# Kernel tuning notes

Measured on AMD Instinct MI355X. Metric: run time of the kernel, lower is better.

The kernel has to match this reference:

```python
import jax, jax.numpy as jnp
import numpy as np

B, S, D, H, OUT = 64, 512, 128, 512, 24


def _linear_params(key, out_dim, in_dim, dtype=jnp.float32):
    kw, kb = jax.random.split(key)
    bound = 1.0 / np.sqrt(in_dim)
    w = jax.random.uniform(kw, (out_dim, in_dim), dtype, -bound, bound)
    b = jax.random.uniform(kb, (out_dim,), dtype, -bound, bound)
    return w, b


def setup_inputs() -> dict:
    key = jax.random.key(0)
    ks = jax.random.split(key, 12)
    inp = {"x": jax.random.normal(ks[0], (B, S, D), jnp.float32)}
    # layer 0 gates: Linear(D+H, H); layer 1 gates: Linear(2H, H)
    names = ["f", "i", "o", "g"]
    for li, in_dim in enumerate([D + H, 2 * H]):
        for gi, n in enumerate(names):
            w, b = _linear_params(ks[1 + li * 4 + gi], H, in_dim)
            inp[f"w{n}{li}"] = w
            inp[f"b{n}{li}"] = b
    inp["fc1_w"], inp["fc1_b"] = _linear_params(ks[9], H, H)
    inp["fc2_w"], inp["fc2_b"] = _linear_params(ks[10], OUT, H)
    return inp


def _cell(inp, h, c, wf, bf, wi, bi, wo, bo, wg, bg):
    comb = jnp.concatenate([inp, h], axis=1)          # [B, in+H]
    f = jax.nn.sigmoid(comb @ wf.T + bf)
    i = jax.nn.sigmoid(comb @ wi.T + bi)
    g = jnp.tanh(comb @ wg.T + bg)
    c = f * c + i * g
    o = jax.nn.sigmoid(comb @ wo.T + bo)
    h = o * jnp.tanh(c)
    return h, c


def reference(x, wf0, bf0, wi0, bi0, wo0, bo0, wg0, bg0,
              wf1, bf1, wi1, bi1, wo1, bo1, wg1, bg1,
              fc1_w, fc1_b, fc2_w, fc2_b):
    layers = ((wf0, bf0, wi0, bi0, wo0, bo0, wg0, bg0),
              (wf1, bf1, wi1, bi1, wo1, bo1, wg1, bg1))
    b, h = x.shape[0], bf0.shape[0]

    def step(carry, xt):
        new = []
        inp = xt
        for params, (hs, cs) in zip(layers, carry):
            hs, cs = _cell(inp, hs, cs, *params)
            inp = hs
            new.append((hs, cs))
        return tuple(new), inp  # last layer's hidden

    init = tuple((jnp.zeros((b, h), x.dtype), jnp.zeros((b, h), x.dtype))
                 for _ in range(len(layers)))
    _, outs = jax.lax.scan(step, init, jnp.swapaxes(x, 0, 1))  # outs: [S, B, H]
    last = outs[-1]                                            # h at final t
    out = last @ fc1_w.T + fc1_b                               # dropout is eval-mode identity
    out = out @ fc2_w.T + fc2_b
    return jax.nn.relu(out)
```

## Files before the change

kernel.cpp:

```cpp
#include <hip/hip_runtime.h>
#include <cmath>

constexpr int kB = 64, kS = 512, kD = 128, kH = 512, kOut = 24;
constexpr int kBlocks = 256, kThreads = 512;
constexpr size_t kBarOffBytes = (size_t)5 * kB * kH * 4;

struct Params {
  const float* x;
  const float* w0[4]; const float* b0[4];
  const float* w1[4]; const float* b1[4];
  const float* fc1w; const float* fc1b;
  const float* fc2w; const float* fc2b;
  float* H0;
  float* H1;
  float* tmp1;
  unsigned* bar;
  float* out;
};

__device__ __forceinline__ float sigmoidf_(float v) {
  return 1.0f / (1.0f + expf(-v));
}

__device__ __forceinline__ void sync_group(unsigned* slots, unsigned* gen,
                                           int myIdx, int n, bool leader,
                                           unsigned r) {
  const int tid = threadIdx.x;
  __syncthreads();
  if (leader) {
    if (tid == 0) {
      __threadfence();
      __hip_atomic_store(slots + myIdx * 16, r + 1, __ATOMIC_RELAXED,
                         __HIP_MEMORY_SCOPE_AGENT);
    }
    unsigned* ps = slots + (tid < n ? tid : 0) * 16;
    for (;;) {
      unsigned v = __hip_atomic_load(ps, __ATOMIC_RELAXED,
                                     __HIP_MEMORY_SCOPE_AGENT);
      if (__syncthreads_and((tid < n) ? (int)(v > r) : 1)) break;
      __builtin_amdgcn_s_sleep(1);
    }
    __threadfence();
    if (tid == 0)
      __hip_atomic_store(gen, r + 1, __ATOMIC_RELAXED,
                         __HIP_MEMORY_SCOPE_AGENT);
    __syncthreads();
  } else {
    if (tid == 0) {
      __threadfence();
      __hip_atomic_store(slots + myIdx * 16, r + 1, __ATOMIC_RELAXED,
                         __HIP_MEMORY_SCOPE_AGENT);
      while (__hip_atomic_load(gen, __ATOMIC_RELAXED,
                               __HIP_MEMORY_SCOPE_AGENT) <= r)
        __builtin_amdgcn_s_sleep(1);
      __threadfence();
    }
    __syncthreads();
  }
}

__global__ void __launch_bounds__(kThreads, 2)
lstm_persistent(Params p) {
  __shared__ float wlds0[16 * 640];
  __shared__ float wlds1[16 * 1024];
  __shared__ float ustg[2][32 * 132];
  __shared__ float gs[512];

  const int tid = threadIdx.x;
  const int bid = blockIdx.x;
  const int cgi = bid >> 1;
  const int bh  = bid & 1;
  const int j0  = cgi * 4;
  const int bbase = bh * 32;

  const int r4 = tid >> 7;
  const int kt = (tid >> 3) & 15;
  const int bg = tid & 7;

  const int k4s  = tid & 31;
  const int bbs0 = tid >> 5;
  const int bbs1 = bbs0 + 16;
  const int bL0 = bbase + bbs0, bL1 = bbase + bbs1;

  unsigned rnd = 0;

  for (int idx = tid; idx < 16 * 160; idx += kThreads) {
    const int row = idx / 160;
    const int k4  = idx - row * 160;
    const float4 v =
        *(const float4*)(p.w0[row >> 2] + (j0 + (row & 3)) * 640 + k4 * 4);
    *(float4*)(wlds0 + row * 640 + k4 * 4) = v;
  }
  for (int idx = tid; idx < 16 * 256; idx += kThreads) {
    const int row = idx >> 8;
    const int k4  = idx & 255;
    const float4 v =
        *(const float4*)(p.w1[row >> 2] + (j0 + (row & 3)) * 1024 + k4 * 4);
    *(float4*)(wlds1 + row * 1024 + k4 * 4) = v;
  }

  if (tid < 128) {
    const int jl = tid >> 5, bb = tid & 31;
    const int b = bbase + bb;
    p.H0[kB * kH + b * kH + j0 + jl] = 0.f;
    p.H1[kB * kH + b * kH + j0 + jl] = 0.f;
  }

  float* H0buf[2] = { p.H0, p.H0 + kB * kH };
  float* H1buf[2] = { p.H1, p.H1 + kB * kH };
  float c0 = 0.f, c1 = 0.f;

  unsigned* domSlots = p.bar + bh * 2048;
  unsigned* domGen   = p.bar + 4096 + bh * 16;
  const bool leader  = (cgi == 0);

  sync_group(domSlots, domGen, cgi, 128, leader, rnd); rnd++;

  auto runPhase = [&](int C, auto&& src, const float* __restrict__ wl,
                      int wstride, const float* const* Bv, float& cs,
                      float* __restrict__ hout) {
    float acc[4][4];
    #pragma unroll
    for (int a = 0; a < 4; ++a)
      #pragma unroll
      for (int q = 0; q < 4; ++q) acc[a][q] = 0.f;

    const float* wr[4];
    #pragma unroll
    for (int rr = 0; rr < 4; ++rr) wr[rr] = wl + (r4 * 4 + rr) * wstride;

    auto compute = [&](int c, const float* __restrict__ ub0) {
      #pragma unroll
      for (int m = 0; m < 2; ++m) {
        const int k4 = m * 16 + kt;
        float4 wv[4], uv[4];
        #pragma unroll
        for (int rr = 0; rr < 4; ++rr)
          wv[rr] = *(const float4*)(wr[rr] + c * 128 + k4 * 4);
        #pragma unroll
        for (int i2 = 0; i2 < 4; ++i2)
          uv[i2] = *(const float4*)(ub0 + (bg + 8 * i2) * 132 + k4 * 4);
        #pragma unroll
        for (int rr = 0; rr < 4; ++rr)
          #pragma unroll
          for (int i2 = 0; i2 < 4; ++i2) {
            acc[rr][i2] = fmaf(wv[rr].x, uv[i2].x, acc[rr][i2]);
            acc[rr][i2] = fmaf(wv[rr].y, uv[i2].y, acc[rr][i2]);
            acc[rr][i2] = fmaf(wv[rr].z, uv[i2].z, acc[rr][i2]);
            acc[rr][i2] = fmaf(wv[rr].w, uv[i2].w, acc[rr][i2]);
          }
      }
    };

    float4 sA0, sA1, sB0, sB1;
    sA0 = *(const float4*)src(0, bL0, k4s);
    sA1 = *(const float4*)src(0, bL1, k4s);
    if (C > 1) {
      sB0 = *(const float4*)src(1, bL0, k4s);
      sB1 = *(const float4*)src(1, bL1, k4s);
    }
    *(float4*)(&ustg[0][bbs0 * 132 + k4s * 4]) = sA0;
    *(float4*)(&ustg[0][bbs1 * 132 + k4s * 4]) = sA1;
    __syncthreads();

    for (int cc = 0; cc < C; cc += 2) {
      {
        const int c = cc;
        if (c + 2 < C) {
          sA0 = *(const float4*)src(c + 2, bL0, k4s);
          sA1 = *(const float4*)src(c + 2, bL1, k4s);
        }
        compute(c, ustg[0]);
        if (c + 1 < C) {
          *(float4*)(&ustg[1][bbs0 * 132 + k4s * 4]) = sB0;
          *(float4*)(&ustg[1][bbs1 * 132 + k4s * 4]) = sB1;
        }
        __syncthreads();
      }
      if (cc + 1 < C) {
        const int c = cc + 1;
        if (c + 2 < C) {
          sB0 = *(const float4*)src(c + 2, bL0, k4s);
          sB1 = *(const float4*)src(c + 2, bL1, k4s);
        }
        compute(c, ustg[1]);
        if (c + 1 < C) {
          *(float4*)(&ustg[0][bbs0 * 132 + k4s * 4]) = sA0;
          *(float4*)(&ustg[0][bbs1 * 132 + k4s * 4]) = sA1;
        }
        __syncthreads();
      }
    }

    float* part = &ustg[0][0];
    #pragma unroll
    for (int rr = 0; rr < 4; ++rr)
      #pragma unroll
      for (int i2 = 0; i2 < 4; ++i2)
        part[kt * 520 + (r4 * 4 + rr) * 32 + bg + 8 * i2] = acc[rr][i2];
    __syncthreads();
    {
      const int row = tid >> 5;
      float s = 0.f;
      #pragma unroll
      for (int q = 0; q < 16; ++q) s += part[q * 520 + tid];
      s += Bv[row >> 2][j0 + (row & 3)];
      gs[tid] = s;
    }
    __syncthreads();
    if (tid < 128) {
      const int jl = tid >> 5, bb = tid & 31;
      const int b = bbase + bb;
      const float fg = sigmoidf_(gs[(0 + jl) * 32 + bb]);
      const float ig = sigmoidf_(gs[(4 + jl) * 32 + bb]);
      const float og = sigmoidf_(gs[(8 + jl) * 32 + bb]);
      const float gg = tanhf(gs[(12 + jl) * 32 + bb]);
      cs = fg * cs + ig * gg;
      hout[b * kH + j0 + jl] = og * tanhf(cs);
    }
  };

  {
    const float* __restrict__ h0prev = H0buf[1];
    auto srcA = [&](int c, int b, int k4) {
      return (c == 0) ? p.x + (b * kS + 0) * kD + k4 * 4
                      : h0prev + b * kH + (c - 1) * 128 + k4 * 4;
    };
    runPhase(5, srcA, wlds0, 640, p.b0, c0, H0buf[0]);
  }
  sync_group(domSlots, domGen, cgi, 128, leader, rnd); rnd++;

  for (int t = 0; t < kS; ++t) {
    {
      const float* __restrict__ h0cur  = H0buf[t & 1];
      const float* __restrict__ h1prev = H1buf[(t + 1) & 1];
      auto srcB = [&](int c, int b, int k4) {
        return (c < 4) ? h0cur + b * kH + c * 128 + k4 * 4
                       : h1prev + b * kH + (c - 4) * 128 + k4 * 4;
      };
      runPhase(8, srcB, wlds1, 1024, p.b1, c1, H1buf[t & 1]);
    }
    if (t < kS - 1) {
      const int tn = t + 1;
      const float* __restrict__ h0prev = H0buf[t & 1];
      auto srcA = [&](int c, int b, int k4) {
        return (c == 0) ? p.x + (b * kS + tn) * kD + k4 * 4
                        : h0prev + b * kH + (c - 1) * 128 + k4 * 4;
      };
      runPhase(5, srcA, wlds0, 640, p.b0, c0, H0buf[(t + 1) & 1]);
    }
    sync_group(domSlots, domGen, cgi, 128, leader, rnd); rnd++;
  }

  const float* h1f = H1buf[(kS - 1) & 1];
  if (tid < 128) {
    const int jl = tid >> 5, bb = tid & 31;
    const int b = bbase + bb;
    const float* __restrict__ wrr = p.fc1w + (j0 + jl) * kH;
    const float* __restrict__ hr = h1f + b * kH;
    float s = p.fc1b[j0 + jl];
    for (int k = 0; k < kH; k += 4) {
      const float4 wv = *(const float4*)(wrr + k);
      const float4 hv = *(const float4*)(hr + k);
      s = fmaf(wv.x, hv.x, s); s = fmaf(wv.y, hv.y, s);
      s = fmaf(wv.z, hv.z, s); s = fmaf(wv.w, hv.w, s);
    }
    p.tmp1[b * kH + j0 + jl] = s;
  }
  sync_group(p.bar + 4224, p.bar + 8320, bid, 256, bid == 0, 0u);

  if (bid < kOut && tid < kB) {
    const int b = tid;
    const float* __restrict__ wrr = p.fc2w + bid * kH;
    const float* __restrict__ tr = p.tmp1 + b * kH;
    float s = p.fc2b[bid];
    for (int k = 0; k < kH; k += 4) {
      const float4 wv = *(const float4*)(wrr + k);
      const float4 tv = *(const float4*)(tr + k);
      s = fmaf(wv.x, tv.x, s); s = fmaf(wv.y, tv.y, s);
      s = fmaf(wv.z, tv.z, s); s = fmaf(wv.w, tv.w, s);
    }
    p.out[b * kOut + bid] = fmaxf(s, 0.f);
  }
}

extern "C" void kernel_launch(void* const* d_in, const int* in_sizes, int n_in,
                              void* d_out, int out_size, void* d_ws, size_t ws_size,
                              hipStream_t stream) {
  (void)in_sizes; (void)n_in; (void)out_size; (void)ws_size;
  Params p;
  p.x = (const float*)d_in[0];
  p.w0[0] = (const float*)d_in[1];  p.b0[0] = (const float*)d_in[2];
  p.w0[1] = (const float*)d_in[3];  p.b0[1] = (const float*)d_in[4];
  p.w0[2] = (const float*)d_in[5];  p.b0[2] = (const float*)d_in[6];
  p.w0[3] = (const float*)d_in[7];  p.b0[3] = (const float*)d_in[8];
  p.w1[0] = (const float*)d_in[9];  p.b1[0] = (const float*)d_in[10];
  p.w1[1] = (const float*)d_in[11]; p.b1[1] = (const float*)d_in[12];
  p.w1[2] = (const float*)d_in[13]; p.b1[2] = (const float*)d_in[14];
  p.w1[3] = (const float*)d_in[15]; p.b1[3] = (const float*)d_in[16];
  p.fc1w = (const float*)d_in[17];  p.fc1b = (const float*)d_in[18];
  p.fc2w = (const float*)d_in[19];  p.fc2b = (const float*)d_in[20];

  float* ws = (float*)d_ws;
  p.H0   = ws;
  p.H1   = ws + 2 * kB * kH;
  p.tmp1 = ws + 4 * kB * kH;
  p.bar  = (unsigned*)((char*)d_ws + kBarOffBytes);
  p.out  = (float*)d_out;

  hipMemsetAsync((char*)d_ws + kBarOffBytes, 0, 36864, stream);

  void* args[] = { &p };
  hipLaunchCooperativeKernel(reinterpret_cast<const void*>(&lstm_persistent),
                             dim3(kBlocks), dim3(kThreads), args, 0, stream);
}
```

Baseline: 14.27 ms.

## Double threads per block and reduce partial sums with wave shuffles

Raises the block size from 512 to 1024 threads. Each thread now covers one k-slice per chunk instead of two, and stages one row instead of two. The cross-k partial sums are first reduced inside each wavefront with xor shuffles, so a 4-way LDS sum replaces the 16-way one. This aims to cut per-thread serial work and LDS reduction traffic on the latency-bound recurrent step. The cost is a larger block with heavier __syncthreads, and the launch_bounds change asks the compiler for 4 such blocks per CU, which tightens register limits and may not be achievable.

```diff
diff --git a/kernel.cpp b/kernel.cpp
--- a/kernel.cpp
+++ b/kernel.cpp
@@ -2,7 +2,7 @@
 #include <cmath>
 
 constexpr int kB = 64, kS = 512, kD = 128, kH = 512, kOut = 24;
-constexpr int kBlocks = 256, kThreads = 512;
+constexpr int kBlocks = 256, kThreads = 1024;
 constexpr size_t kBarOffBytes = (size_t)5 * kB * kH * 4;
 
 struct Params {
@@ -59,7 +59,7 @@
   }
 }
 
-__global__ void __launch_bounds__(kThreads, 2)
+__global__ void __launch_bounds__(kThreads, 4)
 lstm_persistent(Params p) {
   __shared__ float wlds0[16 * 640];
   __shared__ float wlds1[16 * 1024];
@@ -73,14 +73,15 @@
   const int j0  = cgi * 4;
   const int bbase = bh * 32;
 
-  const int r4 = tid >> 7;
-  const int kt = (tid >> 3) & 15;
+  const int r4 = tid >> 8;
+  const int kt = (tid >> 3) & 31;
   const int bg = tid & 7;
-
-  const int k4s  = tid & 31;
-  const int bbs0 = tid >> 5;
-  const int bbs1 = bbs0 + 16;
-  const int bL0 = bbase + bbs0, bL1 = bbase + bbs1;
+  const int lane = tid & 63;
+  const int kh = (tid >> 6) & 3;
+
+  const int k4s = tid & 31;
+  const int bbs = tid >> 5;
+  const int bL  = bbase + bbs;
 
   unsigned rnd = 0;
 
@@ -130,80 +131,72 @@
     for (int rr = 0; rr < 4; ++rr) wr[rr] = wl + (r4 * 4 + rr) * wstride;
 
     auto compute = [&](int c, const float* __restrict__ ub0) {
-      #pragma unroll
-      for (int m = 0; m < 2; ++m) {
-        const int k4 = m * 16 + kt;
-        float4 wv[4], uv[4];
+      float4 wv[4], uv[4];
+      #pragma unroll
+      for (int rr = 0; rr < 4; ++rr)
+        wv[rr] = *(const float4*)(wr[rr] + c * 128 + kt * 4);
+      #pragma unroll
+      for (int i2 = 0; i2 < 4; ++i2)
+        uv[i2] = *(const float4*)(ub0 + (bg + 8 * i2) * 132 + kt * 4);
+      #pragma unroll
+      for (int rr = 0; rr < 4; ++rr)
         #pragma unroll
-        for (int rr = 0; rr < 4; ++rr)
-          wv[rr] = *(const float4*)(wr[rr] + c * 128 + k4 * 4);
-        #pragma unroll
-        for (int i2 = 0; i2 < 4; ++i2)
-          uv[i2] = *(const float4*)(ub0 + (bg + 8 * i2) * 132 + k4 * 4);
-        #pragma unroll
-        for (int rr = 0; rr < 4; ++rr)
-          #pragma unroll
-          for (int i2 = 0; i2 < 4; ++i2) {
-            acc[rr][i2] = fmaf(wv[rr].x, uv[i2].x, acc[rr][i2]);
-            acc[rr][i2] = fmaf(wv[rr].y, uv[i2].y, acc[rr][i2]);
-            acc[rr][i2] = fmaf(wv[rr].z, uv[i2].z, acc[rr][i2]);
-            acc[rr][i2] = fmaf(wv[rr].w, uv[i2].w, acc[rr][i2]);
-          }
-      }
+        for (int i2 = 0; i2 < 4; ++i2) {
+          acc[rr][i2] = fmaf(wv[rr].x, uv[i2].x, acc[rr][i2]);
+          acc[rr][i2] = fmaf(wv[rr].y, uv[i2].y, acc[rr][i2]);
+          acc[rr][i2] = fmaf(wv[rr].z, uv[i2].z, acc[rr][i2]);
+          acc[rr][i2] = fmaf(wv[rr].w, uv[i2].w, acc[rr][i2]);
+        }
     };
 
-    float4 sA0, sA1, sB0, sB1;
-    sA0 = *(const float4*)src(0, bL0, k4s);
-    sA1 = *(const float4*)src(0, bL1, k4s);
-    if (C > 1) {
-      sB0 = *(const float4*)src(1, bL0, k4s);
-      sB1 = *(const float4*)src(1, bL1, k4s);
-    }
-    *(float4*)(&ustg[0][bbs0 * 132 + k4s * 4]) = sA0;
-    *(float4*)(&ustg[0][bbs1 * 132 + k4s * 4]) = sA1;
+    float4 sA, sB;
+    sA = *(const float4*)src(0, bL, k4s);
+    if (C > 1) sB = *(const float4*)src(1, bL, k4s);
+    *(float4*)(&ustg[0][bbs * 132 + k4s * 4]) = sA;
     __syncthreads();
 
     for (int cc = 0; cc < C; cc += 2) {
       {
         const int c = cc;
-        if (c + 2 < C) {
-          sA0 = *(const float4*)src(c + 2, bL0, k4s);
-          sA1 = *(const float4*)src(c + 2, bL1, k4s);
-        }
+        if (c + 2 < C) sA = *(const float4*)src(c + 2, bL, k4s);
         compute(c, ustg[0]);
-        if (c + 1 < C) {
-          *(float4*)(&ustg[1][bbs0 * 132 + k4s * 4]) = sB0;
-          *(float4*)(&ustg[1][bbs1 * 132 + k4s * 4]) = sB1;
-        }
+        if (c + 1 < C)
+          *(float4*)(&ustg[1][bbs * 132 + k4s * 4]) = sB;
         __syncthreads();
       }
       if (cc + 1 < C) {
         const int c = cc + 1;
-        if (c + 2 < C) {
-          sB0 = *(const float4*)src(c + 2, bL0, k4s);
-          sB1 = *(const float4*)src(c + 2, bL1, k4s);
-        }
+        if (c + 2 < C) sB = *(const float4*)src(c + 2, bL, k4s);
         compute(c, ustg[1]);
-        if (c + 1 < C) {
-          *(float4*)(&ustg[0][bbs0 * 132 + k4s * 4]) = sA0;
-          *(float4*)(&ustg[0][bbs1 * 132 + k4s * 4]) = sA1;
-        }
+        if (c + 1 < C)
+          *(float4*)(&ustg[0][bbs * 132 + k4s * 4]) = sA;
         __syncthreads();
       }
     }
 
-    float* part = &ustg[0][0];
     #pragma unroll
     for (int rr = 0; rr < 4; ++rr)
       #pragma unroll
-      for (int i2 = 0; i2 < 4; ++i2)
-        part[kt * 520 + (r4 * 4 + rr) * 32 + bg + 8 * i2] = acc[rr][i2];
-    __syncthreads();
-    {
+      for (int i2 = 0; i2 < 4; ++i2) {
+        float v = acc[rr][i2];
+        v += __shfl_xor(v, 8, 64);
+        v += __shfl_xor(v, 16, 64);
+        v += __shfl_xor(v, 32, 64);
+        acc[rr][i2] = v;
+      }
+    float* part = &ustg[0][0];
+    if ((lane & 56) == 0) {
+      #pragma unroll
+      for (int rr = 0; rr < 4; ++rr)
+        #pragma unroll
+        for (int i2 = 0; i2 < 4; ++i2)
+          part[kh * 512 + (r4 * 4 + rr) * 32 + bg + 8 * i2] = acc[rr][i2];
+    }
+    __syncthreads();
+    if (tid < 512) {
       const int row = tid >> 5;
-      float s = 0.f;
-      #pragma unroll
-      for (int q = 0; q < 16; ++q) s += part[q * 520 + tid];
+      float s = part[tid] + part[512 + tid] + part[1024 + tid] +
+                part[1536 + tid];
       s += Bv[row >> 2][j0 + (row & 3)];
       gs[tid] = s;
     }
```

New measurement: 16.28 ms. +14.0%, slower.

## Give each wave private staging buffers to drop block barriers in gate GEMV

Applied to the files above, without the earlier changes.

Remaps threads so each wave handles four batch rows and stages its own input chunks into a per-wave double-buffered LDS region, removing the per-chunk block-wide __syncthreads. Weight rows in LDS are padded to reduce bank conflicts, and the partial-sum reduction layout is rewritten to match. It relies on intra-wave ordering of LDS writes and reads, and it increases shared memory use.

```diff
diff --git a/kernel.cpp b/kernel.cpp
--- a/kernel.cpp
+++ b/kernel.cpp
@@ -61,9 +61,9 @@
 
 __global__ void __launch_bounds__(kThreads, 2)
 lstm_persistent(Params p) {
-  __shared__ float wlds0[16 * 640];
-  __shared__ float wlds1[16 * 1024];
-  __shared__ float ustg[2][32 * 132];
+  __shared__ float wlds0[16 * 644];
+  __shared__ float wlds1[16 * 1028];
+  __shared__ float arena[8][1066];
   __shared__ float gs[512];
 
   const int tid = threadIdx.x;
@@ -73,14 +73,15 @@
   const int j0  = cgi * 4;
   const int bbase = bh * 32;
 
-  const int r4 = tid >> 7;
-  const int kt = (tid >> 3) & 15;
-  const int bg = tid & 7;
-
-  const int k4s  = tid & 31;
-  const int bbs0 = tid >> 5;
-  const int bbs1 = bbs0 + 16;
-  const int bL0 = bbase + bbs0, bL1 = bbase + bbs1;
+  const int wv_ = tid >> 6;
+  const int l   = tid & 63;
+  const int kt  = l >> 2;
+  const int r4  = l & 3;
+
+  const int row_s  = l >> 4;
+  const int quad_s = l & 15;
+  const int bS = bbase + 4 * wv_ + row_s;
+  float* const uw = &arena[wv_][0];
 
   unsigned rnd = 0;
 
@@ -89,14 +90,14 @@
     const int k4  = idx - row * 160;
     const float4 v =
         *(const float4*)(p.w0[row >> 2] + (j0 + (row & 3)) * 640 + k4 * 4);
-    *(float4*)(wlds0 + row * 640 + k4 * 4) = v;
+    *(float4*)(wlds0 + row * 644 + k4 * 4) = v;
   }
   for (int idx = tid; idx < 16 * 256; idx += kThreads) {
     const int row = idx >> 8;
     const int k4  = idx & 255;
     const float4 v =
         *(const float4*)(p.w1[row >> 2] + (j0 + (row & 3)) * 1024 + k4 * 4);
-    *(float4*)(wlds1 + row * 1024 + k4 * 4) = v;
+    *(float4*)(wlds1 + row * 1028 + k4 * 4) = v;
   }
 
   if (tid < 128) {
@@ -129,82 +130,75 @@
     #pragma unroll
     for (int rr = 0; rr < 4; ++rr) wr[rr] = wl + (r4 * 4 + rr) * wstride;
 
-    auto compute = [&](int c, const float* __restrict__ ub0) {
+    auto compute = [&](int c, const float* __restrict__ ub) {
       #pragma unroll
       for (int m = 0; m < 2; ++m) {
-        const int k4 = m * 16 + kt;
-        float4 wv[4], uv[4];
+        const int q4 = (m * 16 + kt) * 4;
+        float4 wvv[4], uv[4];
         #pragma unroll
         for (int rr = 0; rr < 4; ++rr)
-          wv[rr] = *(const float4*)(wr[rr] + c * 128 + k4 * 4);
+          wvv[rr] = *(const float4*)(wr[rr] + c * 128 + q4);
         #pragma unroll
-        for (int i2 = 0; i2 < 4; ++i2)
-          uv[i2] = *(const float4*)(ub0 + (bg + 8 * i2) * 132 + k4 * 4);
+        for (int b = 0; b < 4; ++b)
+          uv[b] = *(const float4*)(ub + b * 132 + q4);
         #pragma unroll
         for (int rr = 0; rr < 4; ++rr)
           #pragma unroll
-          for (int i2 = 0; i2 < 4; ++i2) {
-            acc[rr][i2] = fmaf(wv[rr].x, uv[i2].x, acc[rr][i2]);
-            acc[rr][i2] = fmaf(wv[rr].y, uv[i2].y, acc[rr][i2]);
-            acc[rr][i2] = fmaf(wv[rr].z, uv[i2].z, acc[rr][i2]);
-            acc[rr][i2] = fmaf(wv[rr].w, uv[i2].w, acc[rr][i2]);
+          for (int b = 0; b < 4; ++b) {
+            acc[rr][b] = fmaf(wvv[rr].x, uv[b].x, acc[rr][b]);
+            acc[rr][b] = fmaf(wvv[rr].y, uv[b].y, acc[rr][b]);
+            acc[rr][b] = fmaf(wvv[rr].z, uv[b].z, acc[rr][b]);
+            acc[rr][b] = fmaf(wvv[rr].w, uv[b].w, acc[rr][b]);
           }
       }
     };
 
-    float4 sA0, sA1, sB0, sB1;
-    sA0 = *(const float4*)src(0, bL0, k4s);
-    sA1 = *(const float4*)src(0, bL1, k4s);
-    if (C > 1) {
-      sB0 = *(const float4*)src(1, bL0, k4s);
-      sB1 = *(const float4*)src(1, bL1, k4s);
-    }
-    *(float4*)(&ustg[0][bbs0 * 132 + k4s * 4]) = sA0;
-    *(float4*)(&ustg[0][bbs1 * 132 + k4s * 4]) = sA1;
-    __syncthreads();
+    float4 sA0 = *(const float4*)src(0, bS, quad_s);
+    float4 sA1 = *(const float4*)src(0, bS, quad_s + 16);
+    float4 sB0, sB1;
+    *(float4*)(uw + row_s * 132 + quad_s * 4) = sA0;
+    *(float4*)(uw + row_s * 132 + (quad_s + 16) * 4) = sA1;
 
     for (int cc = 0; cc < C; cc += 2) {
       {
         const int c = cc;
-        if (c + 2 < C) {
-          sA0 = *(const float4*)src(c + 2, bL0, k4s);
-          sA1 = *(const float4*)src(c + 2, bL1, k4s);
+        if (c + 1 < C) {
+          sB0 = *(const float4*)src(c + 1, bS, quad_s);
+          sB1 = *(const float4*)src(c + 1, bS, quad_s + 16);
         }
-        compute(c, ustg[0]);
+        compute(c, uw);
         if (c + 1 < C) {
-          *(float4*)(&ustg[1][bbs0 * 132 + k4s * 4]) = sB0;
-          *(float4*)(&ustg[1][bbs1 * 132 + k4s * 4]) = sB1;
+          *(float4*)(uw + 528 + row_s * 132 + quad_s * 4) = sB0;
+          *(float4*)(uw + 528 + row_s * 132 + (quad_s + 16) * 4) = sB1;
         }
-        __syncthreads();
       }
       if (cc + 1 < C) {
         const int c = cc + 1;
-        if (c + 2 < C) {
-          sB0 = *(const float4*)src(c + 2, bL0, k4s);
-          sB1 = *(const float4*)src(c + 2, bL1, k4s);
+        if (c + 1 < C) {
+          sA0 = *(const float4*)src(c + 1, bS, quad_s);
+          sA1 = *(const float4*)src(c + 1, bS, quad_s + 16);
         }
-        compute(c, ustg[1]);
+        compute(c, uw + 528);
         if (c + 1 < C) {
-          *(float4*)(&ustg[0][bbs0 * 132 + k4s * 4]) = sA0;
-          *(float4*)(&ustg[0][bbs1 * 132 + k4s * 4]) = sA1;
+          *(float4*)(uw + row_s * 132 + quad_s * 4) = sA0;
+          *(float4*)(uw + row_s * 132 + (quad_s + 16) * 4) = sA1;
         }
-        __syncthreads();
       }
     }
 
-    float* part = &ustg[0][0];
     #pragma unroll
-    for (int rr = 0; rr < 4; ++rr)
-      #pragma unroll
-      for (int i2 = 0; i2 < 4; ++i2)
-        part[kt * 520 + (r4 * 4 + rr) * 32 + bg + 8 * i2] = acc[rr][i2];
+    for (int rr = 0; rr < 4; ++rr) {
+      float4 pv = { acc[rr][0], acc[rr][1], acc[rr][2], acc[rr][3] };
+      *(float4*)(uw + kt * 66 + (r4 * 4 + rr) * 4) = pv;
+    }
     __syncthreads();
     {
-      const int row = tid >> 5;
+      const int rIdx = tid >> 5, bb = tid & 31;
+      const float* pw = &arena[bb >> 2][0];
       float s = 0.f;
       #pragma unroll
-      for (int q = 0; q < 16; ++q) s += part[q * 520 + tid];
-      s += Bv[row >> 2][j0 + (row & 3)];
+      for (int q = 0; q < 16; ++q) s += pw[q * 66 + rIdx * 4 + (bb & 3)];
+      s += Bv[rIdx >> 2][j0 + (rIdx & 3)];
       gs[tid] = s;
     }
     __syncthreads();
@@ -226,7 +220,7 @@
       return (c == 0) ? p.x + (b * kS + 0) * kD + k4 * 4
                       : h0prev + b * kH + (c - 1) * 128 + k4 * 4;
     };
-    runPhase(5, srcA, wlds0, 640, p.b0, c0, H0buf[0]);
+    runPhase(5, srcA, wlds0, 644, p.b0, c0, H0buf[0]);
   }
   sync_group(domSlots, domGen, cgi, 128, leader, rnd); rnd++;
 
@@ -238,7 +232,7 @@
         return (c < 4) ? h0cur + b * kH + c * 128 + k4 * 4
                        : h1prev + b * kH + (c - 4) * 128 + k4 * 4;
       };
-      runPhase(8, srcB, wlds1, 1024, p.b1, c1, H1buf[t & 1]);
+      runPhase(8, srcB, wlds1, 1028, p.b1, c1, H1buf[t & 1]);
     }
     if (t < kS - 1) {
       const int tn = t + 1;
@@ -247,7 +241,7 @@
         return (c == 0) ? p.x + (b * kS + tn) * kD + k4 * 4
                         : h0prev + b * kH + (c - 1) * 128 + k4 * 4;
       };
-      runPhase(5, srcA, wlds0, 640, p.b0, c0, H0buf[(t + 1) & 1]);
+      runPhase(5, srcA, wlds0, 644, p.b0, c0, H0buf[(t + 1) & 1]);
     }
     sync_group(domSlots, domGen, cgi, 128, leader, rnd); rnd++;
   }
@@ -260,10 +254,10 @@
     const float* __restrict__ hr = h1f + b * kH;
     float s = p.fc1b[j0 + jl];
     for (int k = 0; k < kH; k += 4) {
-      const float4 wv = *(const float4*)(wrr + k);
+      const float4 wv4 = *(const float4*)(wrr + k);
       const float4 hv = *(const float4*)(hr + k);
-      s = fmaf(wv.x, hv.x, s); s = fmaf(wv.y, hv.y, s);
-      s = fmaf(wv.z, hv.z, s); s = fmaf(wv.w, hv.w, s);
+      s = fmaf(wv4.x, hv.x, s); s = fmaf(wv4.y, hv.y, s);
+      s = fmaf(wv4.z, hv.z, s); s = fmaf(wv4.w, hv.w, s);
     }
     p.tmp1[b * kH + j0 + jl] = s;
   }
@@ -275,10 +269,10 @@
     const float* __restrict__ tr = p.tmp1 + b * kH;
     float s = p.fc2b[bid];
     for (int k = 0; k < kH; k += 4) {
-      const float4 wv = *(const float4*)(wrr + k);
+      const float4 wv4 = *(const float4*)(wrr + k);
       const float4 tv = *(const float4*)(tr + k);
-      s = fmaf(wv.x, tv.x, s); s = fmaf(wv.y, tv.y, s);
-      s = fmaf(wv.z, tv.z, s); s = fmaf(wv.w, tv.w, s);
+      s = fmaf(wv4.x, tv.x, s); s = fmaf(wv4.y, tv.y, s);
+      s = fmaf(wv4.z, tv.z, s); s = fmaf(wv4.w, tv.w, s);
     }
     p.out[b * kOut + bid] = fmaxf(s, 0.f);
   }
```

Result: slower. 17.95 ms (+25.7%).
